# Performance work log

Measured on AMD Instinct MI355X. Metric: run time of the kernel, lower is better.

## Reference

```python
import jax, jax.numpy as jnp
import numpy as np

B, S, N, C = 128, 512, 64, 1
F = N * C          # flattened feature dim = input_size * n_nodes
H = 512            # hidden_size


def _gru_imputer(x2d, m2d, Wih, Whh, bih, bhh, Wro, bro):
    """Unidirectional 1-step-ahead GRU imputer.
    x2d: [B,S,F] float, m2d: [B,S,F] bool.
    Returns (x_hat [B,S,F], h [B,S,H])."""
    dt = x2d.dtype
    h0 = jnp.zeros((x2d.shape[0], H), dtype=dt)
    xhat0 = h0 @ Wro.T + bro  # readout of initial state (== bro)

    def step(carry, inp):
        h, xhat = carry
        x_t, m_t = inp  # [B,F] float, [B,F] bool
        x_p = jnp.where(m_t, x_t, xhat)
        x_in = jnp.concatenate([x_p, m_t.astype(dt)], axis=-1)  # [B,2F]
        gi = x_in @ Wih.T + bih  # [B,3H]
        gh = h @ Whh.T + bhh     # [B,3H]
        ir, iz, inn = jnp.split(gi, 3, axis=-1)
        hr, hz, hn = jnp.split(gh, 3, axis=-1)
        r = jax.nn.sigmoid(ir + hr)
        z = jax.nn.sigmoid(iz + hz)
        n = jnp.tanh(inn + r * hn)
        h_new = (1.0 - z) * n + z * h
        xhat_new = h_new @ Wro.T + bro
        return (h_new, xhat_new), (h_new, xhat_new)

    xs = (jnp.swapaxes(x2d[:, :-1], 0, 1), jnp.swapaxes(m2d[:, :-1], 0, 1))
    _, (hs, xhats) = jax.lax.scan(step, (h0, xhat0), xs)
    hs = jnp.concatenate([h0[None], hs], axis=0)        # [S,B,H]
    xhats = jnp.concatenate([xhat0[None], xhats], axis=0)  # [S,B,F]
    return jnp.swapaxes(xhats, 0, 1), jnp.swapaxes(hs, 0, 1)


def setup_inputs() -> dict:
    key = jax.random.key(0)
    ks = jax.random.split(key, 16)
    s = 1.0 / np.sqrt(H)
    u = lambda k, shape: jax.random.uniform(k, shape, jnp.float32, -s, s)
    inp = {
        "x": jax.random.normal(ks[0], (B, S, N, C), jnp.float32),
        "mask": jax.random.randint(ks[1], (B, S, N, C), 0, 2).astype(bool),
        # forward-direction RNN params
        "Wih_f": u(ks[2], (3 * H, 2 * F)),
        "Whh_f": u(ks[3], (3 * H, H)),
        "bih_f": u(ks[4], (3 * H,)),
        "bhh_f": u(ks[5], (3 * H,)),
        "Wro_f": u(ks[6], (F, H)),
        "bro_f": u(ks[7], (F,)),
        # backward-direction RNN params
        "Wih_b": u(ks[8], (3 * H, 2 * F)),
        "Whh_b": u(ks[9], (3 * H, H)),
        "bih_b": u(ks[10], (3 * H,)),
        "bhh_b": u(ks[11], (3 * H,)),
        "Wro_b": u(ks[12], (F, H)),
        "bro_b": u(ks[13], (F,)),
        # final bidirectional readout
        "Wout": u(ks[14], (F, 2 * H)),
        "bout": u(ks[15], (F,)),
    }
    return inp


def reference(x, mask, Wih_f, Whh_f, bih_f, bhh_f, Wro_f, bro_f,
              Wih_b, Whh_b, bih_b, bhh_b, Wro_b, bro_b, Wout, bout):
    # rearrange 'b s n c -> b s (n c)'
    x2d = x.reshape(B, S, F)
    m2d = mask.reshape(B, S, F)

    xh_f, h_f = _gru_imputer(x2d, m2d, Wih_f, Whh_f, bih_f, bhh_f, Wro_f, bro_f)
    xh_b, h_b = _gru_imputer(x2d[:, ::-1], m2d[:, ::-1],
                             Wih_b, Whh_b, bih_b, bhh_b, Wro_b, bro_b)
    xh_b = xh_b[:, ::-1]
    h_b = h_b[:, ::-1]

    h = jnp.concatenate([h_f, h_b], axis=-1)  # [B,S,2H]; dropout p=0 -> identity
    x_hat = (h @ Wout.T + bout).reshape(B, S, N, C)
    return (x_hat, xh_f.reshape(B, S, N, C), xh_b.reshape(B, S, N, C))
```

## Files before the change

### kernel.cpp

```cpp
#include <hip/hip_runtime.h>

#define Bx 128
#define Sx 512
#define Fx 64
#define Hx 512
#define Xx 128

#define PARTB_OFF 0ull
#define H_OFF     ((size_t)Bx * Sx * Fx)
#define XHB_OFF   (H_OFF + (size_t)2 * 2 * Hx * Bx)
#define BAR_OFF   (XHB_OFF + (size_t)4 * 2 * Bx * Fx)
#define FLAG_OFF  (BAR_OFF + 4096)

#define LDSW_WHH   0
#define LDSW_XIN   26112
#define LDSW_WRO   (LDSW_XIN + 32 * 160)
#define LDSW_WROS  (LDSW_WRO + 2 * 544)
#define LDSW_WOUTS (LDSW_WROS + 1088)
#define LDSW_HX    (LDSW_WOUTS + 1088)
#define LDSW_TOTAL (LDSW_HX + 512 + 16)

struct BParams {
  const float* x; const void* mask;
  const float* Wih_f; const float* Whh_f; const float* bih_f; const float* bhh_f;
  const float* Wro_f; const float* bro_f;
  const float* Wih_b; const float* Whh_b; const float* bih_b; const float* bhh_b;
  const float* Wro_b; const float* bro_b;
  const float* Wout; const float* bout;
  float* out; float* ws;
};

__global__ void detect_kernel(const unsigned int* mask, float* ws) {
  int* bars = (int*)(ws + BAR_OFF);
  int* flag = (int*)(ws + FLAG_OFF);
  int t = threadIdx.x;
  for (int i = t; i < 4096; i += blockDim.x) bars[i] = 0;
  if (t == 0) *flag = 0;
  __syncthreads();
  unsigned int v = 0;
  for (int i = t; i < 4096; i += blockDim.x) v |= mask[i] & 0xFFFFFF00u;
  if (v) atomicOr(flag, 1);
}

__global__ void init_kernel(float* out, float* partb) {
  size_t i = (size_t)blockIdx.x * blockDim.x + threadIdx.x;
  const size_t n = (size_t)Bx * Sx * Fx / 4;
  if (i < n) {
    ((float4*)out)[i]   = make_float4(0.f, 0.f, 0.f, 0.f);
    ((float4*)partb)[i] = make_float4(0.f, 0.f, 0.f, 0.f);
  }
}

__global__ void combine_kernel(float* out, const float* partb, const float* bout) {
  int i = blockIdx.x * blockDim.x + threadIdx.x;
  out[i] = out[i] + partb[i] + bout[i & 63];
}

__device__ __forceinline__ float sel8(const float* a, int idx) {
  float v = a[0];
#pragma unroll
  for (int i = 1; i < 8; ++i) v = (idx == i) ? a[i] : v;
  return v;
}

__device__ __forceinline__ void st_sys(float* p, float v) {
  __hip_atomic_store(p, v, __ATOMIC_RELAXED, __HIP_MEMORY_SCOPE_SYSTEM);
}
__device__ __forceinline__ void st_sys_i(int* p, int v) {
  __hip_atomic_store(p, v, __ATOMIC_RELAXED, __HIP_MEMORY_SCOPE_SYSTEM);
}

__device__ __forceinline__ void gbar(int* slots, int hs, int nbar) {
  __syncthreads();
  if (threadIdx.x < 64) {
    if (threadIdx.x == 0) st_sys_i(slots + hs * 16, nbar);
    const int* myslot = slots + (threadIdx.x & 31) * 16;
    for (;;) {
      int v = __hip_atomic_load(myslot, __ATOMIC_RELAXED, __HIP_MEMORY_SCOPE_AGENT);
      if (__all(v >= nbar)) break;
      __builtin_amdgcn_s_sleep(1);
    }
    asm volatile("buffer_inv\n\ts_waitcnt vmcnt(0)" ::: "memory");
  }
  __syncthreads();
}

#define GH_STEP(C, JOFF) {                                                   \
  const float* hr = hrd + (size_t)(j0 + jj + (JOFF)) * Bx + bA;              \
  float4 ha  = *(const float4*)(hr);                                         \
  float4 hbv = *(const float4*)(hr + 4);                                     \
  float s0 = w0.C, s1 = w1.C, s2 = w2.C;                                     \
  acc0[0]=fmaf(s0,ha.x,acc0[0]);  acc0[1]=fmaf(s0,ha.y,acc0[1]);             \
  acc0[2]=fmaf(s0,ha.z,acc0[2]);  acc0[3]=fmaf(s0,ha.w,acc0[3]);             \
  acc0[4]=fmaf(s0,hbv.x,acc0[4]); acc0[5]=fmaf(s0,hbv.y,acc0[5]);            \
  acc0[6]=fmaf(s0,hbv.z,acc0[6]); acc0[7]=fmaf(s0,hbv.w,acc0[7]);            \
  acc1[0]=fmaf(s1,ha.x,acc1[0]);  acc1[1]=fmaf(s1,ha.y,acc1[1]);             \
  acc1[2]=fmaf(s1,ha.z,acc1[2]);  acc1[3]=fmaf(s1,ha.w,acc1[3]);             \
  acc1[4]=fmaf(s1,hbv.x,acc1[4]); acc1[5]=fmaf(s1,hbv.y,acc1[5]);            \
  acc1[6]=fmaf(s1,hbv.z,acc1[6]); acc1[7]=fmaf(s1,hbv.w,acc1[7]);            \
  acc3[0]=fmaf(s2,ha.x,acc3[0]);  acc3[1]=fmaf(s2,ha.y,acc3[1]);             \
  acc3[2]=fmaf(s2,ha.z,acc3[2]);  acc3[3]=fmaf(s2,ha.w,acc3[3]);             \
  acc3[4]=fmaf(s2,hbv.x,acc3[4]); acc3[5]=fmaf(s2,hbv.y,acc3[5]);            \
  acc3[6]=fmaf(s2,hbv.z,acc3[6]); acc3[7]=fmaf(s2,hbv.w,acc3[7]); }

__global__ void __launch_bounds__(512, 2)
birnn_main(BParams p) {
  extern __shared__ float lds[];

  const int w   = blockIdx.x;
  const int g   = w & 7;
  const int dir = g >> 2;
  const int bg  = g & 3;
  const int hs  = w >> 3;
  const int b0  = bg * 32;
  const int u0  = hs * 16;
  const int f0  = hs * 2;
  const int tid = threadIdx.x;

  const float* Wih = dir ? p.Wih_b : p.Wih_f;
  const float* Whh = dir ? p.Whh_b : p.Whh_f;
  const float* bih = dir ? p.bih_b : p.bih_f;
  const float* bhh = dir ? p.bhh_b : p.bhh_f;
  const float* Wro = dir ? p.Wro_b : p.Wro_f;
  const float* bro = dir ? p.bro_b : p.bro_f;

  float* hbuf  = p.ws + H_OFF;
  float* xhb4  = p.ws + XHB_OFF;
  int*   slots = (int*)(p.ws + BAR_OFF) + g * 512;
  const int u8f = *(const int*)(p.ws + FLAG_OFF);
  const unsigned char* m8  = (const unsigned char*)p.mask;
  const int*           m32 = (const int*)p.mask;

  float* pout   = dir ? (p.ws + PARTB_OFF) : p.out;
  float* out_xh = p.out + (size_t)(1 + dir) * Bx * Sx * Fx;

  for (int idx = tid; idx < 3 * 16 * 512; idx += 512) {
    int g3 = idx >> 13; int rem = idx & 8191;
    int u = rem >> 9;   int j = rem & 511;
    lds[LDSW_WHH + ((g3 * 16 + u) * 8 + (j >> 6)) * 68 + (j & 63)] =
        Whh[(size_t)(g3 * 512 + u0 + u) * Hx + j];
  }
  for (int idx = tid; idx < 2 * 512; idx += 512) {
    int f = idx >> 9, j = idx & 511;
    lds[LDSW_WRO + f * 544 + (j >> 6) * 68 + (j & 63)] = Wro[(size_t)(f0 + f) * Hx + j];
  }
  for (int idx = tid; idx < 64 * 16; idx += 512) {
    int f = idx >> 4, u = idx & 15;
    lds[LDSW_WROS  + f * 17 + u] = Wro[(size_t)f * Hx + u0 + u];
    lds[LDSW_WOUTS + f * 17 + u] = p.Wout[(size_t)f * (2 * Hx) + dir * Hx + u0 + u];
  }

  if (hs == 0) {
    for (int idx = tid; idx < 32 * 512; idx += 512) {
      int u = idx >> 5, bo = idx & 31;
      st_sys(&hbuf[((size_t)(dir * 2 + 0) * Hx + u) * Bx + b0 + bo], 0.f);
    }
  }
  float bro_own = 0.f;
  if (tid < 64) {
    bro_own = bro[tid];
#pragma unroll
    for (int q = 0; q < 4; ++q)
      st_sys(&xhb4[(((size_t)q * 2 + dir) * Bx + (b0 + hs)) * Fx + tid], bro_own);
  }

  const int jq   = tid & 7;
  const int ulo  = (tid >> 3) & 7;
  const int wv   = tid >> 6;
  const int bsub = wv & 3;
  const int uhi  = wv >> 2;
  const int u    = uhi * 8 + ulo;
  const int bA   = b0 + bsub * 8;
  const int ru   = u0 + u;
  const int j0   = jq * 64;
  const int blo  = (tid >> 3) & 7;
  const int bB   = b0 + (wv & 3) * 8 + blo;
  const int fB   = wv >> 2;
  const int pf   = tid & 63;
  const int pbq  = tid >> 6;

  float4 wih0[4], wih1[4], wih2[4];
#pragma unroll
  for (int q = 0; q < 4; ++q) {
    wih0[q] = *(const float4*)(Wih + (size_t)(0 * 512 + ru) * Xx + jq * 16 + q * 4);
    wih1[q] = *(const float4*)(Wih + (size_t)(1 * 512 + ru) * Xx + jq * 16 + q * 4);
    wih2[q] = *(const float4*)(Wih + (size_t)(2 * 512 + ru) * Xx + jq * 16 + q * 4);
  }
  const float bs_r = bih[ru] + bhh[ru];
  const float bs_z = bih[512 + ru] + bhh[512 + ru];
  const float bs_i = bih[1024 + ru];
  const float bs_h = bhh[1024 + ru];

  const float* w0p = lds + LDSW_WHH + ((0 * 16 + u) * 8 + jq) * 68;
  const float* w1p = lds + LDSW_WHH + ((1 * 16 + u) * 8 + jq) * 68;
  const float* w2p = lds + LDSW_WHH + ((2 * 16 + u) * 8 + jq) * 68;

  float hprev_own = 0.f;

  int nbar = 1;
  gbar(slots, hs, nbar);

  for (int k = 1; k < Sx; ++k) {
    const int pp = k & 1, pr = pp ^ 1;
    const int t_in = dir ? (Sx - k) : (k - 1);
    const int T_k  = dir ? (Sx - 1 - k) : k;
    const int rdq = (k - 1) & 3;
    const int adq = k & 3;
    const int inq = (k + 2) & 3;

    {
      int bl = tid >> 4, sub = tid & 15;
      int b = b0 + bl;
      float* xr = lds + LDSW_XIN + bl * 160 + (sub >> 1) * 20 + (sub & 1) * 8;
      float v[8];
      if (sub < 8) {
        size_t base = ((size_t)b * Sx + t_in) * Fx + sub * 8;
        float4 xa = *(const float4*)(p.x + base);
        float4 xb = *(const float4*)(p.x + base + 4);
        const float* xhp = xhb4 + (((size_t)rdq * 2 + dir) * Bx + b) * Fx + sub * 8;
        float4 ha  = *(const float4*)(xhp);
        float4 hb4 = *(const float4*)(xhp + 4);
        int mi[8];
        if (u8f) {
          unsigned long long mm = *(const unsigned long long*)(m8 + base);
#pragma unroll
          for (int j = 0; j < 8; ++j) mi[j] = (int)((mm >> (8 * j)) & 0xFF);
        } else {
          int4 ma = *(const int4*)(m32 + base);
          int4 mb = *(const int4*)(m32 + base + 4);
          mi[0] = ma.x; mi[1] = ma.y; mi[2] = ma.z; mi[3] = ma.w;
          mi[4] = mb.x; mi[5] = mb.y; mi[6] = mb.z; mi[7] = mb.w;
        }
        v[0] = mi[0] ? xa.x : ha.x;  v[1] = mi[1] ? xa.y : ha.y;
        v[2] = mi[2] ? xa.z : ha.z;  v[3] = mi[3] ? xa.w : ha.w;
        v[4] = mi[4] ? xb.x : hb4.x; v[5] = mi[5] ? xb.y : hb4.y;
        v[6] = mi[6] ? xb.z : hb4.z; v[7] = mi[7] ? xb.w : hb4.w;
      } else {
        size_t base = ((size_t)b * Sx + t_in) * Fx + (sub - 8) * 8;
        if (u8f) {
          unsigned long long mm = *(const unsigned long long*)(m8 + base);
#pragma unroll
          for (int j = 0; j < 8; ++j) v[j] = (float)((mm >> (8 * j)) & 0xFF);
        } else {
          int4 ma = *(const int4*)(m32 + base);
          int4 mb = *(const int4*)(m32 + base + 4);
          v[0] = (float)ma.x; v[1] = (float)ma.y; v[2] = (float)ma.z; v[3] = (float)ma.w;
          v[4] = (float)mb.x; v[5] = (float)mb.y; v[6] = (float)mb.z; v[7] = (float)mb.w;
        }
      }
      *(float4*)(xr)     = make_float4(v[0], v[1], v[2], v[3]);
      *(float4*)(xr + 4) = make_float4(v[4], v[5], v[6], v[7]);
    }
    if (tid < 64) {
      float v = xhb4[(((size_t)rdq * 2 + dir) * Bx + (b0 + hs)) * Fx + tid];
      st_sys(&out_xh[((size_t)(b0 + hs) * Sx + t_in) * Fx + tid], v);
    }
    __syncthreads();

    float acc0[8], acc1[8], acc2[8], acc3[8];
#pragma unroll
    for (int i = 0; i < 8; ++i) { acc0[i] = 0.f; acc1[i] = 0.f; acc2[i] = 0.f; acc3[i] = 0.f; }

    {
      const float* hrd = hbuf + (size_t)(dir * 2 + pr) * Hx * Bx;
#pragma unroll 2
      for (int jj = 0; jj < 64; jj += 4) {
        float4 w0 = *(const float4*)(w0p + jj);
        float4 w1 = *(const float4*)(w1p + jj);
        float4 w2 = *(const float4*)(w2p + jj);
        GH_STEP(x, 0)
        GH_STEP(y, 1)
        GH_STEP(z, 2)
        GH_STEP(w, 3)
      }
    }
    {
      const float* xinb = lds + LDSW_XIN;
#pragma unroll
      for (int q = 0; q < 4; ++q) {
        float4 w0 = wih0[q], w1 = wih1[q], w2 = wih2[q];
        int off = jq * 20 + q * 4;
#pragma unroll
        for (int bb = 0; bb < 8; ++bb) {
          float4 xv = *(const float4*)(xinb + (bsub * 8 + bb) * 160 + off);
          acc0[bb] = fmaf(w0.x, xv.x, acc0[bb]); acc0[bb] = fmaf(w0.y, xv.y, acc0[bb]);
          acc0[bb] = fmaf(w0.z, xv.z, acc0[bb]); acc0[bb] = fmaf(w0.w, xv.w, acc0[bb]);
          acc1[bb] = fmaf(w1.x, xv.x, acc1[bb]); acc1[bb] = fmaf(w1.y, xv.y, acc1[bb]);
          acc1[bb] = fmaf(w1.z, xv.z, acc1[bb]); acc1[bb] = fmaf(w1.w, xv.w, acc1[bb]);
          acc2[bb] = fmaf(w2.x, xv.x, acc2[bb]); acc2[bb] = fmaf(w2.y, xv.y, acc2[bb]);
          acc2[bb] = fmaf(w2.z, xv.z, acc2[bb]); acc2[bb] = fmaf(w2.w, xv.w, acc2[bb]);
        }
      }
    }
#pragma unroll
    for (int m = 1; m <= 4; m <<= 1) {
#pragma unroll
      for (int bb = 0; bb < 8; ++bb) {
        acc0[bb] += __shfl_xor(acc0[bb], m);
        acc1[bb] += __shfl_xor(acc1[bb], m);
        acc2[bb] += __shfl_xor(acc2[bb], m);
        acc3[bb] += __shfl_xor(acc3[bb], m);
      }
    }
    {
      int b = bA + jq;
      float sr  = sel8(acc0, jq);
      float sz  = sel8(acc1, jq);
      float sgi = sel8(acc2, jq);
      float sgh = sel8(acc3, jq);
      float r = 1.f / (1.f + __expf(-(sr + bs_r)));
      float z = 1.f / (1.f + __expf(-(sz + bs_z)));
      float n = tanhf(sgi + bs_i + r * (sgh + bs_h));
      float hn = (1.f - z) * n + z * hprev_own;
      hprev_own = hn;
      st_sys(&hbuf[((size_t)(dir * 2 + pp) * Hx + ru) * Bx + b], hn);
      lds[LDSW_HX + (bsub * 8 + jq) * 16 + u] = hn;
    }
    __syncthreads();

    {
      const float* wros = lds + LDSW_WROS  + pf * 17;
      const float* wout = lds + LDSW_WOUTS + pf * 17;
      float* xq = xhb4 + (((size_t)adq * 2 + dir) * Bx + b0) * Fx;
#pragma unroll
      for (int i = 0; i < 4; ++i) {
        int bl = pbq * 4 + i;
        const float* hx = lds + LDSW_HX + bl * 16;
        float s = 0.f, s2 = 0.f;
#pragma unroll
        for (int uu = 0; uu < 16; ++uu) {
          float hv = hx[uu];
          s  = fmaf(wros[uu], hv, s);
          s2 = fmaf(wout[uu], hv, s2);
        }
        atomicAdd(xq + (size_t)bl * Fx + pf, s);
        atomicAdd(pout + ((size_t)(b0 + bl) * Sx + T_k) * Fx + pf, s2);
      }
    }
    if (tid < 64)
      st_sys(&xhb4[(((size_t)inq * 2 + dir) * Bx + (b0 + hs)) * Fx + tid], bro_own);

    ++nbar;
    gbar(slots, hs, nbar);
  }

  {
    const int ppE = (Sx - 1) & 1;
    const int tE  = dir ? 0 : (Sx - 1);
    const float* hnw  = hbuf + (size_t)(dir * 2 + ppE) * Hx * Bx;
    const float* wroL = lds + LDSW_WRO + fB * 544 + jq * 68;
    const float* hcol = hnw + (size_t)j0 * Bx + bB;
    float ax = 0.f;
#pragma unroll 4
    for (int jj = 0; jj < 64; jj += 4) {
      float4 wx = *(const float4*)(wroL + jj);
      ax = fmaf(wx.x, hcol[(size_t)(jj + 0) * Bx], ax);
      ax = fmaf(wx.y, hcol[(size_t)(jj + 1) * Bx], ax);
      ax = fmaf(wx.z, hcol[(size_t)(jj + 2) * Bx], ax);
      ax = fmaf(wx.w, hcol[(size_t)(jj + 3) * Bx], ax);
    }
#pragma unroll
    for (int m = 1; m <= 4; m <<= 1) ax += __shfl_xor(ax, m);
    const int f = f0 + fB;
    if (jq == 0)
      st_sys(&out_xh[((size_t)bB * Sx + tE) * Fx + f], ax + bro[f]);
  }
}

extern "C" void kernel_launch(void* const* d_in, const int* in_sizes, int n_in,
                              void* d_out, int out_size, void* d_ws, size_t ws_size,
                              hipStream_t stream) {
  (void)in_sizes; (void)n_in; (void)out_size; (void)ws_size;
  float* ws = (float*)d_ws;

  detect_kernel<<<1, 512, 0, stream>>>((const unsigned int*)d_in[1], ws);
  init_kernel<<<(Bx * Sx * Fx / 4 + 255) / 256, 256, 0, stream>>>(
      (float*)d_out, ws + PARTB_OFF);

  BParams p;
  p.x     = (const float*)d_in[0];  p.mask = d_in[1];
  p.Wih_f = (const float*)d_in[2];  p.Whh_f = (const float*)d_in[3];
  p.bih_f = (const float*)d_in[4];  p.bhh_f = (const float*)d_in[5];
  p.Wro_f = (const float*)d_in[6];  p.bro_f = (const float*)d_in[7];
  p.Wih_b = (const float*)d_in[8];  p.Whh_b = (const float*)d_in[9];
  p.bih_b = (const float*)d_in[10]; p.bhh_b = (const float*)d_in[11];
  p.Wro_b = (const float*)d_in[12]; p.bro_b = (const float*)d_in[13];
  p.Wout  = (const float*)d_in[14]; p.bout  = (const float*)d_in[15];
  p.out   = (float*)d_out;
  p.ws    = ws;

  hipFuncSetAttribute(reinterpret_cast<const void*>(birnn_main),
                      hipFuncAttributeMaxDynamicSharedMemorySize,
                      (int)(LDSW_TOTAL * sizeof(float)));
  void* args[] = { (void*)&p };
  hipLaunchCooperativeKernel(reinterpret_cast<void*>(birnn_main),
                             dim3(256), dim3(512), args,
                             (unsigned)(LDSW_TOTAL * sizeof(float)), stream);

  combine_kernel<<<dim3(Bx * Sx * Fx / 256), dim3(256), 0, stream>>>(
      (float*)d_out, ws + PARTB_OFF, (const float*)d_in[15]);
}
```

Baseline: 18.40 ms.

## Split recurrent GRU work across 512 smaller blocks with 64-way grid barrier

Adds a v2 persistent cooperative kernel that launches 512 blocks of 256 threads, each owning 8 hidden units instead of 16. The r and z recurrent weights stay in LDS while the n-gate weights are streamed from global memory, and the grid barrier now waits on 64 slots. Per-timestep xhat output is written by designated owner blocks rather than computed in a separate pass. The aim is to spread the serial per-step work over more CUs and cut per-block latency, at the cost of a wider barrier, more atomics and extra global weight reads. The old kernel remains as a fallback if occupancy is below two blocks per CU.

```diff
diff --git a/kernel.cpp b/kernel.cpp
--- a/kernel.cpp
+++ b/kernel.cpp
@@ -10,7 +10,7 @@
 #define H_OFF     ((size_t)Bx * Sx * Fx)
 #define XHB_OFF   (H_OFF + (size_t)2 * 2 * Hx * Bx)
 #define BAR_OFF   (XHB_OFF + (size_t)4 * 2 * Bx * Fx)
-#define FLAG_OFF  (BAR_OFF + 4096)
+#define FLAG_OFF  (BAR_OFF + 8192)
 
 #define LDSW_WHH   0
 #define LDSW_XIN   26112
@@ -19,6 +19,13 @@
 #define LDSW_WOUTS (LDSW_WROS + 1088)
 #define LDSW_HX    (LDSW_WOUTS + 1088)
 #define LDSW_TOTAL (LDSW_HX + 512 + 16)
+
+#define V2_WHH    0
+#define V2_XIN    8704
+#define V2_WROS   (V2_XIN + 5120)
+#define V2_WOUTS  (V2_WROS + 576)
+#define V2_HX     (V2_WOUTS + 576)
+#define V2_TOTAL  (V2_HX + 256 + 16)
 
 struct BParams {
   const float* x; const void* mask;
@@ -34,7 +41,7 @@
   int* bars = (int*)(ws + BAR_OFF);
   int* flag = (int*)(ws + FLAG_OFF);
   int t = threadIdx.x;
-  for (int i = t; i < 4096; i += blockDim.x) bars[i] = 0;
+  for (int i = t; i < 8192; i += blockDim.x) bars[i] = 0;
   if (t == 0) *flag = 0;
   __syncthreads();
   unsigned int v = 0;
@@ -70,11 +77,26 @@
   __hip_atomic_store(p, v, __ATOMIC_RELAXED, __HIP_MEMORY_SCOPE_SYSTEM);
 }
 
-__device__ __forceinline__ void gbar(int* slots, int hs, int nbar) {
+__device__ __forceinline__ void gbar32(int* slots, int hs, int nbar) {
   __syncthreads();
   if (threadIdx.x < 64) {
     if (threadIdx.x == 0) st_sys_i(slots + hs * 16, nbar);
     const int* myslot = slots + (threadIdx.x & 31) * 16;
+    for (;;) {
+      int v = __hip_atomic_load(myslot, __ATOMIC_RELAXED, __HIP_MEMORY_SCOPE_AGENT);
+      if (__all(v >= nbar)) break;
+      __builtin_amdgcn_s_sleep(1);
+    }
+    asm volatile("buffer_inv\n\ts_waitcnt vmcnt(0)" ::: "memory");
+  }
+  __syncthreads();
+}
+
+__device__ __forceinline__ void gbar64(int* slots, int hs, int nbar) {
+  __syncthreads();
+  if (threadIdx.x < 64) {
+    if (threadIdx.x == 0) st_sys_i(slots + hs * 16, nbar);
+    const int* myslot = slots + threadIdx.x * 16;
     for (;;) {
       int v = __hip_atomic_load(myslot, __ATOMIC_RELAXED, __HIP_MEMORY_SCOPE_AGENT);
       if (__all(v >= nbar)) break;
@@ -104,7 +126,7 @@
   acc3[6]=fmaf(s2,hbv.z,acc3[6]); acc3[7]=fmaf(s2,hbv.w,acc3[7]); }
 
 __global__ void __launch_bounds__(512, 2)
-birnn_main(BParams p) {
+birnn_r15(BParams p) {
   extern __shared__ float lds[];
 
   const int w   = blockIdx.x;
@@ -114,7 +136,6 @@
   const int hs  = w >> 3;
   const int b0  = bg * 32;
   const int u0  = hs * 16;
-  const int f0  = hs * 2;
   const int tid = threadIdx.x;
 
   const float* Wih = dir ? p.Wih_b : p.Wih_f;
@@ -142,7 +163,8 @@
   }
   for (int idx = tid; idx < 2 * 512; idx += 512) {
     int f = idx >> 9, j = idx & 511;
-    lds[LDSW_WRO + f * 544 + (j >> 6) * 68 + (j & 63)] = Wro[(size_t)(f0 + f) * Hx + j];
+    lds[LDSW_WRO + f * 544 + (j >> 6) * 68 + (j & 63)] =
+        Wro[(size_t)(hs * 2 + f) * Hx + j];
   }
   for (int idx = tid; idx < 64 * 16; idx += 512) {
     int f = idx >> 4, u = idx & 15;
@@ -162,6 +184,8 @@
 #pragma unroll
     for (int q = 0; q < 4; ++q)
       st_sys(&xhb4[(((size_t)q * 2 + dir) * Bx + (b0 + hs)) * Fx + tid], bro_own);
+    int T0 = dir ? (Sx - 1) : 0;
+    st_sys(&out_xh[((size_t)(b0 + hs) * Sx + T0) * Fx + tid], bro_own);
   }
 
   const int jq   = tid & 7;
@@ -198,7 +222,7 @@
   float hprev_own = 0.f;
 
   int nbar = 1;
-  gbar(slots, hs, nbar);
+  gbar32(slots, hs, nbar);
 
   for (int k = 1; k < Sx; ++k) {
     const int pp = k & 1, pr = pp ^ 1;
@@ -341,7 +365,7 @@
       st_sys(&xhb4[(((size_t)inq * 2 + dir) * Bx + (b0 + hs)) * Fx + tid], bro_own);
 
     ++nbar;
-    gbar(slots, hs, nbar);
+    gbar32(slots, hs, nbar);
   }
 
   {
@@ -361,9 +385,293 @@
     }
 #pragma unroll
     for (int m = 1; m <= 4; m <<= 1) ax += __shfl_xor(ax, m);
-    const int f = f0 + fB;
+    const int f = hs * 2 + fB;
     if (jq == 0)
       st_sys(&out_xh[((size_t)bB * Sx + tE) * Fx + f], ax + bro[f]);
+  }
+}
+
+__global__ void __launch_bounds__(256, 2)
+birnn_v2(BParams p) {
+  extern __shared__ float lds[];
+
+  const int w   = blockIdx.x;
+  const int g   = w & 7;
+  const int dir = g >> 2;
+  const int bg  = g & 3;
+  const int hs  = w >> 3;
+  const int b0  = bg * 32;
+  const int u0  = hs * 8;
+  const int tid = threadIdx.x;
+
+  const float* Wih = dir ? p.Wih_b : p.Wih_f;
+  const float* Whh = dir ? p.Whh_b : p.Whh_f;
+  const float* bih = dir ? p.bih_b : p.bih_f;
+  const float* bhh = dir ? p.bhh_b : p.bhh_f;
+  const float* Wro = dir ? p.Wro_b : p.Wro_f;
+  const float* bro = dir ? p.bro_b : p.bro_f;
+
+  float* hbuf  = p.ws + H_OFF;
+  float* xhb4  = p.ws + XHB_OFF;
+  int*   slots = (int*)(p.ws + BAR_OFF) + g * 1024;
+  const int u8f = *(const int*)(p.ws + FLAG_OFF);
+  const unsigned char* m8  = (const unsigned char*)p.mask;
+  const int*           m32 = (const int*)p.mask;
+
+  float* pout   = dir ? (p.ws + PARTB_OFF) : p.out;
+  float* out_xh = p.out + (size_t)(1 + dir) * Bx * Sx * Fx;
+
+  for (int idx = tid; idx < 2 * 8 * 512; idx += 256) {
+    int g3 = idx >> 12; int rem = idx & 4095;
+    int u = rem >> 9;   int j = rem & 511;
+    lds[V2_WHH + ((g3 * 8 + u) * 8 + (j >> 6)) * 68 + (j & 63)] =
+        Whh[(size_t)(g3 * 512 + u0 + u) * Hx + j];
+  }
+  for (int idx = tid; idx < 64 * 8; idx += 256) {
+    int f = idx >> 3, uu = idx & 7;
+    lds[V2_WROS  + f * 9 + uu] = Wro[(size_t)f * Hx + u0 + uu];
+    lds[V2_WOUTS + f * 9 + uu] = p.Wout[(size_t)f * (2 * Hx) + dir * Hx + u0 + uu];
+  }
+
+  if (hs == 0) {
+    for (int idx = tid; idx < 32 * 512; idx += 256) {
+      int u = idx >> 5, bo = idx & 31;
+      st_sys(&hbuf[((size_t)(dir * 2 + 0) * Hx + u) * Bx + b0 + bo], 0.f);
+    }
+  }
+  const int ownb  = ((hs & 1) == 0);
+  const int b_own = b0 + (hs >> 1);
+  float bro_own = 0.f;
+  if (tid < 64) {
+    bro_own = bro[tid];
+    if (ownb) {
+#pragma unroll
+      for (int q = 0; q < 4; ++q)
+        st_sys(&xhb4[(((size_t)q * 2 + dir) * Bx + b_own) * Fx + tid], bro_own);
+      int T0 = dir ? (Sx - 1) : 0;
+      st_sys(&out_xh[((size_t)b_own * Sx + T0) * Fx + tid], bro_own);
+    }
+  }
+
+  const int jq   = tid & 7;
+  const int ulo  = (tid >> 3) & 7;
+  const int wv   = tid >> 6;
+  const int bsub = wv;
+  const int bA   = b0 + bsub * 8;
+  const int ru   = u0 + ulo;
+  const int j0   = jq * 64;
+  const int blo  = (tid >> 3) & 7;
+  const int bB   = b0 + wv * 8 + blo;
+  const int pf   = tid & 63;
+  const int pbq  = tid >> 6;
+  const int sbl  = tid >> 3;
+  const int ssub = tid & 7;
+  const int b_st = b0 + sbl;
+
+  float4 wih0[4], wih1[4], wih2[4];
+#pragma unroll
+  for (int q = 0; q < 4; ++q) {
+    wih0[q] = *(const float4*)(Wih + (size_t)(0 * 512 + ru) * Xx + jq * 16 + q * 4);
+    wih1[q] = *(const float4*)(Wih + (size_t)(1 * 512 + ru) * Xx + jq * 16 + q * 4);
+    wih2[q] = *(const float4*)(Wih + (size_t)(2 * 512 + ru) * Xx + jq * 16 + q * 4);
+  }
+  const float bs_r = bih[ru] + bhh[ru];
+  const float bs_z = bih[512 + ru] + bhh[512 + ru];
+  const float bs_i = bih[1024 + ru];
+  const float bs_h = bhh[1024 + ru];
+
+  const float* w0p = lds + V2_WHH + ((0 * 8 + ulo) * 8 + jq) * 68;
+  const float* w1p = lds + V2_WHH + ((1 * 8 + ulo) * 8 + jq) * 68;
+  const float* w2g = Whh + (size_t)(2 * 512 + ru) * Hx + j0;
+
+  float hprev_own = 0.f;
+
+  int nbar = 1;
+  gbar64(slots, hs, nbar);
+
+  for (int k = 1; k < Sx; ++k) {
+    const int pp = k & 1, pr = pp ^ 1;
+    const int t_in = dir ? (Sx - k) : (k - 1);
+    const int T_k  = dir ? (Sx - 1 - k) : k;
+    const int rdq = (k - 1) & 3;
+    const int adq = k & 3;
+    const int inq = (k + 2) & 3;
+
+    {
+      float* xr = lds + V2_XIN + sbl * 160 + ssub * 20;
+      if (ssub < 4) {
+        size_t base = ((size_t)b_st * Sx + t_in) * Fx + ssub * 16;
+        float4 x0 = *(const float4*)(p.x + base);
+        float4 x1 = *(const float4*)(p.x + base + 4);
+        float4 x2 = *(const float4*)(p.x + base + 8);
+        float4 x3 = *(const float4*)(p.x + base + 12);
+        const float* xhp = xhb4 + (((size_t)rdq * 2 + dir) * Bx + b_st) * Fx + ssub * 16;
+        float4 h0 = *(const float4*)(xhp);
+        float4 h1 = *(const float4*)(xhp + 4);
+        float4 h2 = *(const float4*)(xhp + 8);
+        float4 h3 = *(const float4*)(xhp + 12);
+        int mi[16];
+        if (u8f) {
+          unsigned long long ma = *(const unsigned long long*)(m8 + base);
+          unsigned long long mb = *(const unsigned long long*)(m8 + base + 8);
+#pragma unroll
+          for (int j = 0; j < 8; ++j) { mi[j] = (int)((ma >> (8 * j)) & 0xFF);
+                                        mi[8 + j] = (int)((mb >> (8 * j)) & 0xFF); }
+        } else {
+          int4 q0 = *(const int4*)(m32 + base);
+          int4 q1 = *(const int4*)(m32 + base + 4);
+          int4 q2 = *(const int4*)(m32 + base + 8);
+          int4 q3 = *(const int4*)(m32 + base + 12);
+          mi[0]=q0.x; mi[1]=q0.y; mi[2]=q0.z; mi[3]=q0.w;
+          mi[4]=q1.x; mi[5]=q1.y; mi[6]=q1.z; mi[7]=q1.w;
+          mi[8]=q2.x; mi[9]=q2.y; mi[10]=q2.z; mi[11]=q2.w;
+          mi[12]=q3.x; mi[13]=q3.y; mi[14]=q3.z; mi[15]=q3.w;
+        }
+        *(float4*)(xr + 0)  = make_float4(mi[0] ? x0.x : h0.x, mi[1] ? x0.y : h0.y,
+                                          mi[2] ? x0.z : h0.z, mi[3] ? x0.w : h0.w);
+        *(float4*)(xr + 4)  = make_float4(mi[4] ? x1.x : h1.x, mi[5] ? x1.y : h1.y,
+                                          mi[6] ? x1.z : h1.z, mi[7] ? x1.w : h1.w);
+        *(float4*)(xr + 8)  = make_float4(mi[8] ? x2.x : h2.x, mi[9] ? x2.y : h2.y,
+                                          mi[10] ? x2.z : h2.z, mi[11] ? x2.w : h2.w);
+        *(float4*)(xr + 12) = make_float4(mi[12] ? x3.x : h3.x, mi[13] ? x3.y : h3.y,
+                                          mi[14] ? x3.z : h3.z, mi[15] ? x3.w : h3.w);
+      } else {
+        size_t base = ((size_t)b_st * Sx + t_in) * Fx + (ssub - 4) * 16;
+        float v[16];
+        if (u8f) {
+          unsigned long long ma = *(const unsigned long long*)(m8 + base);
+          unsigned long long mb = *(const unsigned long long*)(m8 + base + 8);
+#pragma unroll
+          for (int j = 0; j < 8; ++j) { v[j] = (float)((ma >> (8 * j)) & 0xFF);
+                                        v[8 + j] = (float)((mb >> (8 * j)) & 0xFF); }
+        } else {
+          int4 q0 = *(const int4*)(m32 + base);
+          int4 q1 = *(const int4*)(m32 + base + 4);
+          int4 q2 = *(const int4*)(m32 + base + 8);
+          int4 q3 = *(const int4*)(m32 + base + 12);
+          v[0]=(float)q0.x; v[1]=(float)q0.y; v[2]=(float)q0.z; v[3]=(float)q0.w;
+          v[4]=(float)q1.x; v[5]=(float)q1.y; v[6]=(float)q1.z; v[7]=(float)q1.w;
+          v[8]=(float)q2.x; v[9]=(float)q2.y; v[10]=(float)q2.z; v[11]=(float)q2.w;
+          v[12]=(float)q3.x; v[13]=(float)q3.y; v[14]=(float)q3.z; v[15]=(float)q3.w;
+        }
+        *(float4*)(xr + 0)  = make_float4(v[0], v[1], v[2], v[3]);
+        *(float4*)(xr + 4)  = make_float4(v[4], v[5], v[6], v[7]);
+        *(float4*)(xr + 8)  = make_float4(v[8], v[9], v[10], v[11]);
+        *(float4*)(xr + 12) = make_float4(v[12], v[13], v[14], v[15]);
+      }
+    }
+    if (ownb && tid < 64) {
+      float v = xhb4[(((size_t)rdq * 2 + dir) * Bx + b_own) * Fx + tid];
+      st_sys(&out_xh[((size_t)b_own * Sx + t_in) * Fx + tid], v);
+    }
+    __syncthreads();
+
+    float acc0[8], acc1[8], acc2[8], acc3[8];
+#pragma unroll
+    for (int i = 0; i < 8; ++i) { acc0[i] = 0.f; acc1[i] = 0.f; acc2[i] = 0.f; acc3[i] = 0.f; }
+
+    {
+      const float* hrd = hbuf + (size_t)(dir * 2 + pr) * Hx * Bx;
+#pragma unroll 4
+      for (int jj = 0; jj < 64; jj += 4) {
+        float4 w0 = *(const float4*)(w0p + jj);
+        float4 w1 = *(const float4*)(w1p + jj);
+        float4 w2 = *(const float4*)(w2g + jj);
+        GH_STEP(x, 0)
+        GH_STEP(y, 1)
+        GH_STEP(z, 2)
+        GH_STEP(w, 3)
+      }
+    }
+    {
+      const float* xinb = lds + V2_XIN;
+#pragma unroll
+      for (int q = 0; q < 4; ++q) {
+        float4 w0 = wih0[q], w1 = wih1[q], w2 = wih2[q];
+        int off = jq * 20 + q * 4;
+#pragma unroll
+        for (int bb = 0; bb < 8; ++bb) {
+          float4 xv = *(const float4*)(xinb + (bsub * 8 + bb) * 160 + off);
+          acc0[bb] = fmaf(w0.x, xv.x, acc0[bb]); acc0[bb] = fmaf(w0.y, xv.y, acc0[bb]);
+          acc0[bb] = fmaf(w0.z, xv.z, acc0[bb]); acc0[bb] = fmaf(w0.w, xv.w, acc0[bb]);
+          acc1[bb] = fmaf(w1.x, xv.x, acc1[bb]); acc1[bb] = fmaf(w1.y, xv.y, acc1[bb]);
+          acc1[bb] = fmaf(w1.z, xv.z, acc1[bb]); acc1[bb] = fmaf(w1.w, xv.w, acc1[bb]);
+          acc2[bb] = fmaf(w2.x, xv.x, acc2[bb]); acc2[bb] = fmaf(w2.y, xv.y, acc2[bb]);
+          acc2[bb] = fmaf(w2.z, xv.z, acc2[bb]); acc2[bb] = fmaf(w2.w, xv.w, acc2[bb]);
+        }
+      }
+    }
+#pragma unroll
+    for (int m = 1; m <= 4; m <<= 1) {
+#pragma unroll
+      for (int bb = 0; bb < 8; ++bb) {
+        acc0[bb] += __shfl_xor(acc0[bb], m);
+        acc1[bb] += __shfl_xor(acc1[bb], m);
+        acc2[bb] += __shfl_xor(acc2[bb], m);
+        acc3[bb] += __shfl_xor(acc3[bb], m);
+      }
+    }
+    {
+      int b = bA + jq;
+      float sr  = sel8(acc0, jq);
+      float sz  = sel8(acc1, jq);
+      float sgi = sel8(acc2, jq);
+      float sgh = sel8(acc3, jq);
+      float r = 1.f / (1.f + __expf(-(sr + bs_r)));
+      float z = 1.f / (1.f + __expf(-(sz + bs_z)));
+      float n = tanhf(sgi + bs_i + r * (sgh + bs_h));
+      float hn = (1.f - z) * n + z * hprev_own;
+      hprev_own = hn;
+      st_sys(&hbuf[((size_t)(dir * 2 + pp) * Hx + ru) * Bx + b], hn);
+      lds[V2_HX + (bsub * 8 + jq) * 8 + ulo] = hn;
+    }
+    __syncthreads();
+
+    {
+      const float* wros = lds + V2_WROS  + pf * 9;
+      const float* wout = lds + V2_WOUTS + pf * 9;
+      float* xq = xhb4 + (((size_t)adq * 2 + dir) * Bx + b0) * Fx;
+#pragma unroll
+      for (int i = 0; i < 8; ++i) {
+        int bl = pbq * 8 + i;
+        const float* hx = lds + V2_HX + bl * 8;
+        float s = 0.f, s2 = 0.f;
+#pragma unroll
+        for (int uu = 0; uu < 8; ++uu) {
+          float hv = hx[uu];
+          s  = fmaf(wros[uu], hv, s);
+          s2 = fmaf(wout[uu], hv, s2);
+        }
+        atomicAdd(xq + (size_t)bl * Fx + pf, s);
+        atomicAdd(pout + ((size_t)(b0 + bl) * Sx + T_k) * Fx + pf, s2);
+      }
+    }
+    if (ownb && tid < 64)
+      st_sys(&xhb4[(((size_t)inq * 2 + dir) * Bx + b_own) * Fx + tid], bro_own);
+
+    ++nbar;
+    gbar64(slots, hs, nbar);
+  }
+
+  {
+    const int ppE = (Sx - 1) & 1;
+    const int tE  = dir ? 0 : (Sx - 1);
+    const float* hnw  = hbuf + (size_t)(dir * 2 + ppE) * Hx * Bx;
+    const float* wroG = Wro + (size_t)hs * Hx + j0;
+    const float* hcol = hnw + (size_t)j0 * Bx + bB;
+    float ax = 0.f;
+#pragma unroll 4
+    for (int jj = 0; jj < 64; jj += 4) {
+      float4 wx = *(const float4*)(wroG + jj);
+      ax = fmaf(wx.x, hcol[(size_t)(jj + 0) * Bx], ax);
+      ax = fmaf(wx.y, hcol[(size_t)(jj + 1) * Bx], ax);
+      ax = fmaf(wx.z, hcol[(size_t)(jj + 2) * Bx], ax);
+      ax = fmaf(wx.w, hcol[(size_t)(jj + 3) * Bx], ax);
+    }
+#pragma unroll
+    for (int m = 1; m <= 4; m <<= 1) ax += __shfl_xor(ax, m);
+    if (jq == 0)
+      st_sys(&out_xh[((size_t)bB * Sx + tE) * Fx + hs], ax + bro[hs]);
   }
 }
 
@@ -388,14 +696,24 @@
   p.Wout  = (const float*)d_in[14]; p.bout  = (const float*)d_in[15];
   p.out   = (float*)d_out;
   p.ws    = ws;
-
-  hipFuncSetAttribute(reinterpret_cast<const void*>(birnn_main),
-                      hipFuncAttributeMaxDynamicSharedMemorySize,
-                      (int)(LDSW_TOTAL * sizeof(float)));
   void* args[] = { (void*)&p };
-  hipLaunchCooperativeKernel(reinterpret_cast<void*>(birnn_main),
-                             dim3(256), dim3(512), args,
-                             (unsigned)(LDSW_TOTAL * sizeof(float)), stream);
+
+  int nb = 0;
+  hipError_t qe = hipOccupancyMaxActiveBlocksPerMultiprocessor(
+      &nb, reinterpret_cast<const void*>(birnn_v2), 256,
+      (size_t)(V2_TOTAL * sizeof(float)));
+  if (qe == hipSuccess && nb >= 2) {
+    hipLaunchCooperativeKernel(reinterpret_cast<void*>(birnn_v2),
+                               dim3(512), dim3(256), args,
+                               (unsigned)(V2_TOTAL * sizeof(float)), stream);
+  } else {
+    hipFuncSetAttribute(reinterpret_cast<const void*>(birnn_r15),
+                        hipFuncAttributeMaxDynamicSharedMemorySize,
+                        (int)(LDSW_TOTAL * sizeof(float)));
+    hipLaunchCooperativeKernel(reinterpret_cast<void*>(birnn_r15),
+                               dim3(256), dim3(512), args,
+                               (unsigned)(LDSW_TOTAL * sizeof(float)), stream);
+  }
 
   combine_kernel<<<dim3(Bx * Sx * Fx / 256), dim3(256), 0, stream>>>(
       (float*)d_out, ws + PARTB_OFF, (const float*)d_in[15]);
```

After: 18.38 ms. No clear change (-0.1%).
